# Optimization experiments

Hardware: AMD Instinct MI355X
Metric: run time of the kernel (lower is better)

## Reference

```python
import jax, jax.numpy as jnp
import numpy as np

B, T, E, NH, VOCAB, MULT = 1, 1024, 768, 12, 32000, 32
N = E * MULT // NH  # 2048
LN_EPS = 1e-5


def setup_inputs() -> dict:
    key = jax.random.key(0)
    ks = jax.random.split(key, 6)
    return {
        "idx": jax.random.randint(ks[0], (B, T), 0, VOCAB),
        "embed": jax.random.normal(ks[1], (VOCAB, E), jnp.float32) * 0.02,
        "encoder": jax.random.normal(ks[2], (NH, E, N), jnp.float32) * 0.02,
        "encoder_v": jax.random.normal(ks[3], (NH, E, N), jnp.float32) * 0.02,
        "decoder": jax.random.normal(ks[4], (NH * N, E), jnp.float32) * 0.02,
        "lm_head": jax.random.normal(ks[5], (VOCAB, E), jnp.float32) * 0.02,
        "ln_w": jnp.ones((E,), jnp.float32),
        "ln_b": jnp.zeros((E,), jnp.float32),
        "n_layer": 6,
    }


def reference(idx, embed, encoder, encoder_v, decoder, lm_head, ln_w, ln_b, n_layer):
    nh, e, n = encoder.shape
    t = idx.shape[1]
    dec = decoder.reshape(nh, n, e)  # flatten order (h, n) -> h*N + n

    def ln(x):
        m = jnp.mean(x, axis=-1, keepdims=True)
        v = jnp.mean(jnp.square(x - m), axis=-1, keepdims=True)
        return (x - m) * jax.lax.rsqrt(v + LN_EPS) * ln_w + ln_b

    causal = jnp.tril(jnp.ones((t, t), bool))  # [T, T]
    scale = 1.0 / np.sqrt(n).astype(np.float32)

    x = ln(embed[idx])  # [B, T, E]  (the unsqueezed head dim broadcasts; keep it squeezed)
    for _ in range(n_layer):
        # encoder projection + ReLU: [B,T,E] x [H,E,N] -> [B,H,T,N]
        x_sparse = jax.nn.relu(jnp.einsum("bte,hen->bhtn", x, encoder))
        # hand-rolled causal attention, Q=K=x_sparse, V=x (broadcast over heads)
        scores = jnp.einsum("bhqn,bhkn->bhqk", x_sparse, x_sparse) * scale
        scores = jnp.where(causal, scores, -jnp.inf)
        attn = jax.nn.softmax(scores, axis=-1)
        y = jnp.einsum("bhqk,bke->bhqe", attn, x)  # [B,H,T,E]
        y = ln(y)
        y_sparse = jax.nn.relu(jnp.einsum("bhte,hen->bhtn", y, encoder_v))
        xy = x_sparse * y_sparse  # [B,H,T,N]; dropout p=0 -> identity
        y_mlp = jnp.einsum("bhtn,hne->bte", xy, dec)  # decoder matmul
        x = ln(x + ln(y_mlp))
    logits = jnp.einsum("bte,ve->btv", x, lm_head)
    return logits
```

## Files before the change

kernel.cpp:

```cpp
#include <hip/hip_runtime.h>

typedef unsigned short u16;
typedef short bf16x8 __attribute__((ext_vector_type(8)));
typedef float f32x4 __attribute__((ext_vector_type(4)));
typedef u16 u16x4 __attribute__((ext_vector_type(4)));

#define TT     1024
#define EE     768
#define NHH    12
#define ND     2048
#define VOC    32000
#define HNN    24576
#define NLAYER 6
#define LN_EPS 1e-5f
#define SPLITK 16

__device__ __forceinline__ float b2f(u16 u){
  unsigned int x = ((unsigned int)u) << 16; float f; __builtin_memcpy(&f, &x, 4); return f;
}
__device__ __forceinline__ u16 f2b(float f){
  unsigned int x; __builtin_memcpy(&x, &f, 4);
  x = x + 0x7fffu + ((x >> 16) & 1u);
  return (u16)(x >> 16);
}

__device__ __forceinline__ void gload16(const void* g, void* lds){
  __builtin_amdgcn_global_load_lds(
      (const __attribute__((address_space(1))) unsigned int*)g,
      (__attribute__((address_space(3))) unsigned int*)(unsigned int)(unsigned long long)lds,
      16, 0, 0);
}

__device__ __forceinline__ bf16x8 ldsr(unsigned addr){
  bf16x8 r;
  asm volatile("ds_read_b128 %0, %1" : "=v"(r) : "v"(addr));
  return r;
}

__device__ __forceinline__ void blk_sum2(float& a, float& b){
  #pragma unroll
  for (int o = 32; o > 0; o >>= 1){ a += __shfl_down(a, o); b += __shfl_down(b, o); }
  __shared__ float sa[4], sb[4];
  int lane = threadIdx.x & 63, wid = threadIdx.x >> 6;
  __syncthreads();
  if (lane == 0){ sa[wid] = a; sb[wid] = b; }
  __syncthreads();
  a = (sa[0] + sa[1]) + (sa[2] + sa[3]);
  b = (sb[0] + sb[1]) + (sb[2] + sb[3]);
}
__device__ __forceinline__ float blk_max(float v){
  #pragma unroll
  for (int o = 32; o > 0; o >>= 1) v = fmaxf(v, __shfl_down(v, o));
  __shared__ float sm[4];
  int lane = threadIdx.x & 63, wid = threadIdx.x >> 6;
  __syncthreads();
  if (lane == 0) sm[wid] = v;
  __syncthreads();
  return fmaxf(fmaxf(sm[0], sm[1]), fmaxf(sm[2], sm[3]));
}
__device__ __forceinline__ float blk_sum(float v){
  #pragma unroll
  for (int o = 32; o > 0; o >>= 1) v += __shfl_down(v, o);
  __shared__ float ss[4];
  int lane = threadIdx.x & 63, wid = threadIdx.x >> 6;
  __syncthreads();
  if (lane == 0) ss[wid] = v;
  __syncthreads();
  return (ss[0] + ss[1]) + (ss[2] + ss[3]);
}

__global__ void transpose_f2b(const float* __restrict__ in, long sIn,
                              u16* __restrict__ out, long sOut, int R, int Cc){
  __shared__ float tile[32][33];
  int z = blockIdx.z;
  in  += (long)z * sIn;
  out += (long)z * sOut;
  int c0 = blockIdx.x * 32, r0 = blockIdx.y * 32;
  int lx = threadIdx.x & 31, ly = threadIdx.x >> 5;
  #pragma unroll
  for (int i = 0; i < 32; i += 8)
    tile[ly + i][lx] = in[(long)(r0 + ly + i) * Cc + (c0 + lx)];
  __syncthreads();
  #pragma unroll
  for (int i = 0; i < 32; i += 8)
    out[(long)(c0 + ly + i) * R + (r0 + lx)] = f2b(tile[lx][ly + i]);
}

__global__ void conv_f2b(const float* __restrict__ in, u16* __restrict__ out){
  long i = ((long)blockIdx.x * 256 + threadIdx.x) * 4;
  float4 v = *(const float4*)(in + i);
  u16x4 o; o.x = f2b(v.x); o.y = f2b(v.y); o.z = f2b(v.z); o.w = f2b(v.w);
  *(u16x4*)(out + i) = o;
}

__global__ void embed_ln(const int* __restrict__ idx, const float* __restrict__ emb,
                         const float* __restrict__ w, const float* __restrict__ b,
                         float* __restrict__ xf, u16* __restrict__ xb, u16* __restrict__ xT){
  int t = blockIdx.x, tid = threadIdx.x;
  const float* src = emb + (long)idx[t] * EE;
  float v[3];
  #pragma unroll
  for (int j = 0; j < 3; j++) v[j] = src[tid + j * 256];
  float s = v[0] + v[1] + v[2];
  float s2 = v[0]*v[0] + v[1]*v[1] + v[2]*v[2];
  blk_sum2(s, s2);
  float m  = s * (1.0f / EE);
  float var = s2 * (1.0f / EE) - m * m;
  float rs = rsqrtf(var + LN_EPS);
  #pragma unroll
  for (int j = 0; j < 3; j++){
    int e = tid + j * 256;
    float o = (v[j] - m) * rs * w[e] + b[e];
    xf[(long)t * EE + e] = o;
    u16 ob = f2b(o);
    xb[(long)t * EE + e] = ob;
    xT[(long)e * TT + t] = ob;
  }
}

__global__ void ln_rows(const float* __restrict__ in, u16* __restrict__ out,
                        const float* __restrict__ w, const float* __restrict__ b){
  long row = blockIdx.x; int tid = threadIdx.x;
  const float* src = in + row * EE;
  float v[3];
  #pragma unroll
  for (int j = 0; j < 3; j++) v[j] = src[tid + j * 256];
  float s = v[0] + v[1] + v[2];
  float s2 = v[0]*v[0] + v[1]*v[1] + v[2]*v[2];
  blk_sum2(s, s2);
  float m = s * (1.0f / EE);
  float var = s2 * (1.0f / EE) - m * m;
  float rs = rsqrtf(var + LN_EPS);
  #pragma unroll
  for (int j = 0; j < 3; j++){
    int e = tid + j * 256;
    out[row * EE + e] = f2b((v[j] - m) * rs * w[e] + b[e]);
  }
}

__global__ void softmax_rows(const float* __restrict__ scores, u16* __restrict__ attn){
  int q = blockIdx.x, h = blockIdx.y, tid = threadIdx.x;
  const float* srow = scores + ((long)h * TT + q) * TT;
  u16* arow = attn + ((long)h * TT + q) * TT;
  const int len = q + 1;
  const int pad = (q + 128) & ~127;
  float v[4];
  float mx = -1e30f;
  #pragma unroll
  for (int j = 0; j < 4; j++){
    int i = tid + j * 256;
    if (i < len){ v[j] = srow[i]; mx = fmaxf(mx, v[j]); }
  }
  mx = blk_max(mx);
  float s = 0.f;
  #pragma unroll
  for (int j = 0; j < 4; j++){
    int i = tid + j * 256;
    if (i < len){ v[j] = __expf(v[j] - mx); s += v[j]; }
  }
  float inv = 1.0f / blk_sum(s);
  #pragma unroll
  for (int j = 0; j < 4; j++){
    int i = tid + j * 256;
    if (i < pad){
      u16 o = 0;
      if (i < len) o = f2b(v[j] * inv);
      arow[i] = o;
    }
  }
}

template<int P>
__global__ void residual_ln(const u16* __restrict__ part, const float* __restrict__ xin,
                            float* __restrict__ xf, u16* __restrict__ xb, u16* __restrict__ xT,
                            const float* __restrict__ w, const float* __restrict__ b){
  int t = blockIdx.x, tid = threadIdx.x;
  float g[3];
  #pragma unroll
  for (int j = 0; j < 3; j++){
    int e = tid + j * 256;
    float s = 0.f;
    #pragma unroll
    for (int pp = 0; pp < P; pp++) s += b2f(part[((long)pp * TT + t) * EE + e]);
    g[j] = s;
  }
  float s = g[0] + g[1] + g[2], s2 = g[0]*g[0] + g[1]*g[1] + g[2]*g[2];
  blk_sum2(s, s2);
  float m = s * (1.0f / EE), var = s2 * (1.0f / EE) - m * m;
  float rs = rsqrtf(var + LN_EPS);
  float hh[3];
  #pragma unroll
  for (int j = 0; j < 3; j++){
    int e = tid + j * 256;
    hh[j] = xin[(long)t * EE + e] + ((g[j] - m) * rs * w[e] + b[e]);
  }
  s = hh[0] + hh[1] + hh[2]; s2 = hh[0]*hh[0] + hh[1]*hh[1] + hh[2]*hh[2];
  blk_sum2(s, s2);
  m = s * (1.0f / EE); var = s2 * (1.0f / EE) - m * m; rs = rsqrtf(var + LN_EPS);
  #pragma unroll
  for (int j = 0; j < 3; j++){
    int e = tid + j * 256;
    float o = (hh[j] - m) * rs * w[e] + b[e];
    xf[(long)t * EE + e] = o;
    u16 ob = f2b(o);
    xb[(long)t * EE + e] = ob;
    xT[(long)e * TT + t] = ob;
  }
}

template<int EPI>
__global__ __launch_bounds__(512, 2)
void g8(const u16* __restrict__ Ab, long sA,
        const u16* __restrict__ Bb, long sB,
        void* __restrict__ Cb, long sC,
        int grid_m, int grid_mn,
        int K, int lda, int ldb, int ldc, float scale,
        const u16* __restrict__ Mul, long sMul, int ldmul){
  __shared__ __align__(16) u16 S[69632];

  const int nwg = gridDim.x, orig = blockIdx.x;
  const int q = nwg >> 3, r = nwg & 7, xcd = orig & 7;
  const int wgid = (xcd < r ? xcd*(q+1) : r*(q+1) + (xcd - r)*q) + (orig >> 3);
  const int z   = wgid / grid_mn;
  const int rem = wgid - z*grid_mn;
  const int nb  = rem / grid_m;
  const int mb  = rem - nb*grid_m;
  const int m0 = mb*256, n0 = nb*256;
  const int tid = threadIdx.x, lane = tid & 63, wid = tid >> 6;

  if (EPI == 2 && n0 > m0 + 255) return;

  const u16* A = Ab + (long)z*sA;
  const u16* B = Bb + (long)z*sB;

  const int rS = wid*16 + (lane >> 2);
  const int cS = (((lane & 3) ^ ((rS >> 1) & 3)) << 3);
  const u16* gA = A + (long)(m0 + rS)*lda + cS;
  const u16* gB = B + (long)(n0 + rS)*ldb + cS;

  char* Sb = (char*)&S[0];
  const unsigned db0 = 0, db1 = 65536u, scr = 131072u;
  auto issue = [&](const u16* src, unsigned dstOff){
    gload16(src, Sb + dstOff + (unsigned)wid*1024u);
  };

  const int wr = wid >> 2, wc = wid & 3;
  const int fr = lane & 15, fk = lane >> 4;
  const unsigned base = (unsigned)(unsigned long long)Sb;
  unsigned aOff[8], bOff[4];
  #pragma unroll
  for (int mi = 0; mi < 8; mi++){
    int row = wr*128 + mi*16 + fr;
    aOff[mi] = (unsigned)(row*64 + ((fk ^ ((row >> 1) & 3)) << 4));
  }
  #pragma unroll
  for (int ni = 0; ni < 4; ni++){
    int row = wc*64 + ni*16 + fr;
    bOff[ni] = 32768u + (unsigned)(row*64 + ((fk ^ ((row >> 1) & 3)) << 4));
  }

  const int NT = K >> 6;
  const long lda128 = (long)128*lda, ldb128 = (long)128*ldb;

  f32x4 acc[8][4] = {};

  issue(gA,              db0);          issue(gA + lda128,          db0 + 8192u);
  issue(gB,              db0+32768u);   issue(gB + ldb128,          db0 + 40960u);
  issue(gA + 32,         db0+16384u);   issue(gA + 32 + lda128,     db0 + 24576u);
  issue(gB + 32,         db0+49152u);   issue(gB + 32 + ldb128,     db0 + 57344u);
  issue(gA + 64,         db1);          issue(gA + 64 + lda128,     db1 + 8192u);
  issue(gB + 64,         db1+32768u);   issue(gB + 64 + ldb128,     db1 + 40960u);
  asm volatile("s_waitcnt vmcnt(8)" ::: "memory");
  __builtin_amdgcn_s_barrier();
  __builtin_amdgcn_sched_barrier(0);

  for (int t = 0; t < NT; t++){
    const unsigned cur = (t & 1) ? db1 : db0;
    const unsigned oth = (t & 1) ? db0 : db1;
    const bool v1 = (t + 1 < NT), v2 = (t + 2 < NT);
    const long k1 = (long)(v1 ? t + 1 : 0) * 64;
    const long k2 = (long)(v2 ? t + 2 : 0) * 64;
    const unsigned d1A = v1 ? oth + 16384u : scr;
    const unsigned d1B = v1 ? oth + 49152u : scr;
    const unsigned d2A = v2 ? cur           : scr;
    const unsigned d2B = v2 ? cur + 32768u  : scr;
    bf16x8 a[4], b[4];

    #pragma unroll
    for (int ni = 0; ni < 4; ni++) b[ni] = ldsr(base + cur + bOff[ni]);
    #pragma unroll
    for (int u = 0; u < 4; u++)    a[u]  = ldsr(base + cur + aOff[u]);
    issue(gA + k1 + 32, d1A); issue(gA + k1 + 32 + lda128, d1A + 8192u);
    __builtin_amdgcn_s_barrier();
    asm volatile("s_waitcnt lgkmcnt(0)" ::: "memory");
    __builtin_amdgcn_sched_barrier(0);
    __builtin_amdgcn_s_setprio(1);
    #pragma unroll
    for (int u = 0; u < 4; u++)
      #pragma unroll
      for (int ni = 0; ni < 4; ni++)
        acc[u][ni] = __builtin_amdgcn_mfma_f32_16x16x32_bf16(a[u], b[ni], acc[u][ni], 0, 0, 0);
    __builtin_amdgcn_s_setprio(0);
    __builtin_amdgcn_s_barrier();
    __builtin_amdgcn_sched_barrier(0);

    #pragma unroll
    for (int u = 0; u < 4; u++) a[u] = ldsr(base + cur + aOff[4 + u]);
    issue(gB + k1 + 32, d1B); issue(gB + k1 + 32 + ldb128, d1B + 8192u);
    __builtin_amdgcn_s_barrier();
    asm volatile("s_waitcnt lgkmcnt(0)" ::: "memory");
    __builtin_amdgcn_sched_barrier(0);
    __builtin_amdgcn_s_setprio(1);
    #pragma unroll
    for (int u = 0; u < 4; u++)
      #pragma unroll
      for (int ni = 0; ni < 4; ni++)
        acc[4+u][ni] = __builtin_amdgcn_mfma_f32_16x16x32_bf16(a[u], b[ni], acc[4+u][ni], 0, 0, 0);
    __builtin_amdgcn_s_setprio(0);
    asm volatile("s_waitcnt vmcnt(8)" ::: "memory");
    __builtin_amdgcn_s_barrier();
    __builtin_amdgcn_sched_barrier(0);

    #pragma unroll
    for (int ni = 0; ni < 4; ni++) b[ni] = ldsr(base + cur + bOff[ni] + 16384u);
    #pragma unroll
    for (int u = 0; u < 4; u++)    a[u]  = ldsr(base + cur + aOff[u] + 16384u);
    issue(gA + k2, d2A); issue(gA + k2 + lda128, d2A + 8192u);
    __builtin_amdgcn_s_barrier();
    asm volatile("s_waitcnt lgkmcnt(0)" ::: "memory");
    __builtin_amdgcn_sched_barrier(0);
    __builtin_amdgcn_s_setprio(1);
    #pragma unroll
    for (int u = 0; u < 4; u++)
      #pragma unroll
      for (int ni = 0; ni < 4; ni++)
        acc[u][ni] = __builtin_amdgcn_mfma_f32_16x16x32_bf16(a[u], b[ni], acc[u][ni], 0, 0, 0);
    __builtin_amdgcn_s_setprio(0);
    __builtin_amdgcn_s_barrier();
    __builtin_amdgcn_sched_barrier(0);

    #pragma unroll
    for (int u = 0; u < 4; u++) a[u] = ldsr(base + cur + aOff[4 + u] + 16384u);
    issue(gB + k2, d2B); issue(gB + k2 + ldb128, d2B + 8192u);
    __builtin_amdgcn_s_barrier();
    asm volatile("s_waitcnt lgkmcnt(0)" ::: "memory");
    __builtin_amdgcn_sched_barrier(0);
    __builtin_amdgcn_s_setprio(1);
    #pragma unroll
    for (int u = 0; u < 4; u++)
      #pragma unroll
      for (int ni = 0; ni < 4; ni++)
        acc[4+u][ni] = __builtin_amdgcn_mfma_f32_16x16x32_bf16(a[u], b[ni], acc[4+u][ni], 0, 0, 0);
    __builtin_amdgcn_s_setprio(0);
    asm volatile("s_waitcnt vmcnt(8)" ::: "memory");
    __builtin_amdgcn_s_barrier();
    __builtin_amdgcn_sched_barrier(0);
  }
  asm volatile("s_waitcnt vmcnt(0)" ::: "memory");

  const int er = (lane >> 4) * 4, ec = lane & 15;
  #pragma unroll
  for (int mi = 0; mi < 8; mi++){
    #pragma unroll
    for (int ni = 0; ni < 4; ni++){
      #pragma unroll
      for (int j = 0; j < 4; j++){
        int row = m0 + wr*128 + mi*16 + er + j;
        int col = n0 + wc*64 + ni*16 + ec;
        float v = acc[mi][ni][j];
        if (EPI == 0){
          ((float*)Cb + (long)z * sC)[(long)row * ldc + col] = v;
        } else if (EPI == 1){
          v = v > 0.f ? v : 0.f;
          ((u16*)Cb + (long)z * sC)[(long)row * ldc + col] = f2b(v);
        } else if (EPI == 2){
          ((float*)Cb + (long)z * sC)[(long)row * ldc + col] = v * scale;
        } else {
          v = v > 0.f ? v : 0.f;
          float mfv = b2f((Mul + (long)z * sMul)[(long)row * ldmul + col]);
          ((u16*)Cb + (long)z * sC)[(long)row * ldc + col] = f2b(v * mfv);
        }
      }
    }
  }
}

template<int EPI, bool CCLAMP>
__global__ __launch_bounds__(256, 2)
void gemmw(const u16* __restrict__ Ab, long sA,
           const u16* __restrict__ Bb, long sB,
           void* __restrict__ Cb, long sC,
           int grid_m, int grid_mn,
           int K, int lda, int ldb, int ldc){
  constexpr unsigned BUFB = 24576u;
  __shared__ __align__(16) u16 S[3 * 12288];

  const int nwg = gridDim.x, orig = blockIdx.x;
  const int q = nwg >> 3, r = nwg & 7, xcd = orig & 7;
  const int wgid = (xcd < r ? xcd*(q+1) : r*(q+1) + (xcd - r)*q) + (orig >> 3);
  const int z   = wgid / grid_mn;
  const int rem = wgid - z*grid_mn;
  const int nb  = rem / grid_m;
  const int mb  = rem - nb*grid_m;
  const int m0 = mb*128, n0 = nb*256;
  const int tid = threadIdx.x, lane = tid & 63, wid = tid >> 6;

  const u16* A = Ab + (long)z*sA;
  const u16* B = Bb + (long)z*sB;

  const int rS = tid >> 2;
  const int cS = (((tid & 3) ^ ((rS >> 1) & 3)) << 3);
  const u16* gA[2]; const u16* gB[4];
  #pragma unroll
  for (int i = 0; i < 2; i++) gA[i] = A + (long)(m0 + i*64 + rS)*lda + cS;
  #pragma unroll
  for (int i = 0; i < 4; i++) gB[i] = B + (long)(n0 + i*64 + rS)*ldb + cS;

  char* Sb = (char*)&S[0];
  auto stage = [&](int kt, unsigned bB){
    const int ko = kt << 5;
    gload16(gA[0] + ko, Sb + bB +          wid*1024u);
    gload16(gA[1] + ko, Sb + bB +  4096u + wid*1024u);
    #pragma unroll
    for (int i = 0; i < 4; i++)
      gload16(gB[i] + ko, Sb + bB + 8192u + i*4096u + wid*1024u);
  };

  const int wr = wid >> 1, wc = wid & 1;
  const int fr = lane & 15, fk = lane >> 4;
  const unsigned base = (unsigned)(unsigned long long)Sb;
  unsigned aAd[4], bAd[8];
  #pragma unroll
  for (int mi = 0; mi < 4; mi++){
    int row = wr*64 + mi*16 + fr;
    aAd[mi] = base + (unsigned)(row*64 + ((fk ^ ((row >> 1) & 3)) << 4));
  }
  #pragma unroll
  for (int ni = 0; ni < 8; ni++){
    int row = wc*128 + ni*16 + fr;
    bAd[ni] = base + 8192u + (unsigned)(row*64 + ((fk ^ ((row >> 1) & 3)) << 4));
  }

  const int Keff = CCLAMP ? (m0 + 128 < K ? m0 + 128 : K) : K;
  const int NT = Keff >> 5;
  const int s0 = (mb*13 + nb*7 + z*5) % NT;

  f32x4 acc[4][8] = {};

  int p1 = s0 + 1; if (p1 >= NT) p1 -= NT;
  stage(s0, 0);
  stage(p1, BUFB);
  asm volatile("s_waitcnt vmcnt(6)" ::: "memory");
  __builtin_amdgcn_s_barrier();
  __builtin_amdgcn_sched_barrier(0);

  unsigned rbB = 0, wbB = 2u*BUFB;
  for (int t = 0; t < NT; t++){
    int nx = (t + 2 < NT) ? t + 2 : NT - 1;
    int ph = s0 + nx; if (ph >= NT) ph -= NT;
    stage(ph, wbB);
    bf16x8 afr[4], bfr[8];
    #pragma unroll
    for (int ni = 0; ni < 8; ni++) bfr[ni] = ldsr(bAd[ni] + rbB);
    #pragma unroll
    for (int mi = 0; mi < 4; mi++) afr[mi] = ldsr(aAd[mi] + rbB);
    __builtin_amdgcn_s_barrier();
    asm volatile("s_waitcnt lgkmcnt(0)" ::: "memory");
    __builtin_amdgcn_sched_barrier(0);
    __builtin_amdgcn_s_setprio(1);
    #pragma unroll
    for (int mi = 0; mi < 4; mi++)
      #pragma unroll
      for (int ni = 0; ni < 8; ni++)
        acc[mi][ni] = __builtin_amdgcn_mfma_f32_16x16x32_bf16(afr[mi], bfr[ni], acc[mi][ni], 0, 0, 0);
    __builtin_amdgcn_s_setprio(0);
    __builtin_amdgcn_sched_barrier(0);
    asm volatile("s_waitcnt vmcnt(6)" ::: "memory");
    __builtin_amdgcn_s_barrier();
    __builtin_amdgcn_sched_barrier(0);
    unsigned tmp = rbB; rbB += BUFB; if (rbB == 3u*BUFB) rbB = 0;
    wbB = tmp;
  }
  asm volatile("s_waitcnt vmcnt(0)" ::: "memory");

  const int er = (lane >> 4) * 4, ec = lane & 15;
  #pragma unroll
  for (int mi = 0; mi < 4; mi++){
    #pragma unroll
    for (int ni = 0; ni < 8; ni++){
      #pragma unroll
      for (int j = 0; j < 4; j++){
        int row = m0 + wr*64 + mi*16 + er + j;
        int col = n0 + wc*128 + ni*16 + ec;
        float v = acc[mi][ni][j];
        if (EPI == 0){
          ((float*)Cb + (long)z * sC)[(long)row * ldc + col] = v;
        } else {
          ((u16*)Cb + (long)z * sC)[(long)row * ldc + col] = f2b(v);
        }
      }
    }
  }
}

extern "C" void kernel_launch(void* const* d_in, const int* in_sizes, int n_in,
                              void* d_out, int out_size, void* d_ws, size_t ws_size,
                              hipStream_t stream){
  (void)in_sizes; (void)n_in; (void)out_size; (void)ws_size;
  const int*   idx     = (const int*)  d_in[0];
  const float* embed   = (const float*)d_in[1];
  const float* encoder = (const float*)d_in[2];
  const float* encv    = (const float*)d_in[3];
  const float* decoder = (const float*)d_in[4];
  const float* lm_head = (const float*)d_in[5];
  const float* ln_w    = (const float*)d_in[6];
  const float* ln_b    = (const float*)d_in[7];
  float* out = (float*)d_out;

  char* p = (char*)d_ws;
  auto take = [&](size_t n){ char* r = p; p += (n + 255) & ~(size_t)255; return r; };
  u16*   encT  = (u16*)  take((size_t)NHH * ND * EE * 2);
  u16*   encvT = (u16*)  take((size_t)NHH * ND * EE * 2);
  u16*   decT  = (u16*)  take((size_t)EE * HNN * 2);
  u16*   lmhB  = (u16*)  take((size_t)VOC * EE * 2);
  float* xf    = (float*)take((size_t)TT * EE * 4);
  u16*   xb    = (u16*)  take((size_t)TT * EE * 2);
  u16*   xT    = (u16*)  take((size_t)EE * TT * 2);
  u16*   xs    = (u16*)  take((size_t)NHH * TT * ND * 2);
  char*  big   =         take((size_t)NHH * TT * TT * 4);
  u16*   attn  = (u16*)  take((size_t)NHH * TT * TT * 2);
  u16*   yb    = (u16*)  take((size_t)NHH * TT * EE * 2);
  take((size_t)8 * TT * EE * 4);
  float* scores = (float*)big;
  float* yf     = (float*)big;
  u16*   xy     = (u16*)big;
  u16*   part   = attn;

  dim3 blk(256, 1, 1);

  transpose_f2b<<<dim3(ND / 32, EE / 32, NHH), blk, 0, stream>>>(encoder, (long)EE * ND, encT,  (long)ND * EE, EE, ND);
  transpose_f2b<<<dim3(ND / 32, EE / 32, NHH), blk, 0, stream>>>(encv,    (long)EE * ND, encvT, (long)ND * EE, EE, ND);
  transpose_f2b<<<dim3(EE / 32, HNN / 32, 1),  blk, 0, stream>>>(decoder, 0, decT, 0, HNN, EE);
  conv_f2b<<<dim3((VOC * EE) / 1024, 1, 1), blk, 0, stream>>>(lm_head, lmhB);

  embed_ln<<<dim3(TT, 1, 1), blk, 0, stream>>>(idx, embed, ln_w, ln_b, xf, xb, xT);

  const float scl = 0.022097086912079608f;

  for (int L = 0; L < NLAYER; ++L){
    g8<1><<<dim3(4*8*NHH), dim3(512), 0, stream>>>(
        xb, 0, encT, (long)ND * EE, xs, (long)TT * ND,
        4, 32, EE, EE, EE, ND, 0.f, (const u16*)0, 0, 0);
    g8<2><<<dim3(4*4*NHH), dim3(512), 0, stream>>>(
        xs, (long)TT * ND, xs, (long)TT * ND, scores, (long)TT * TT,
        4, 16, ND, ND, ND, TT, scl, (const u16*)0, 0, 0);
    softmax_rows<<<dim3(TT, NHH, 1), blk, 0, stream>>>(scores, attn);
    gemmw<0,true><<<dim3(8*3*NHH), blk, 0, stream>>>(
        attn, (long)TT * TT, xT, 0, yf, (long)TT * EE,
        8, 24, TT, TT, TT, EE);
    ln_rows<<<dim3(NHH * TT, 1, 1), blk, 0, stream>>>(yf, yb, ln_w, ln_b);
    g8<3><<<dim3(4*8*NHH), dim3(512), 0, stream>>>(
        yb, (long)TT * EE, encvT, (long)ND * EE, xy, (long)ND,
        4, 32, EE, EE, EE, HNN, 0.f, xs, (long)TT * ND, ND);
    gemmw<4,false><<<dim3(8*3*SPLITK), blk, 0, stream>>>(
        xy, (long)(HNN / SPLITK), decT, (long)(HNN / SPLITK), part, (long)TT * EE,
        8, 24, HNN / SPLITK, HNN, HNN, EE);
    residual_ln<SPLITK><<<dim3(TT, 1, 1), blk, 0, stream>>>(part, xf, xf, xb, xT, ln_w, ln_b);
  }

  g8<0><<<dim3(4*125), dim3(512), 0, stream>>>(
      xb, 0, lmhB, 0, out, 0,
      4, 500, EE, EE, EE, VOC, 0.f, (const u16*)0, 0, 0);
}
```

Baseline: 1.964 ms.

## Store scores and attention outputs in bf16 and transpose x with a tiled kernel

Attention scores are now written by the score GEMM as bf16 instead of fp32, and softmax reads bf16. The attn@x GEMM writes bf16 through the EPI 4 path, and ln_rows reads it, halving that intermediate's traffic. The strided scattered xT writes in embed_ln and residual_ln are replaced by a separate LDS-tiled transpose kernel. This cuts memory bandwidth on the large per-head intermediates, but it adds precision loss in the scores before softmax and in the pre-LN activations, plus one extra launch per layer.

```diff
diff --git a/kernel.cpp b/kernel.cpp
--- a/kernel.cpp
+++ b/kernel.cpp
@@ -93,9 +93,22 @@
   *(u16x4*)(out + i) = o;
 }
 
+__global__ void xpose(const u16* __restrict__ in, u16* __restrict__ out){
+  __shared__ u16 t[64][65];
+  int e0 = blockIdx.x * 64, t0 = blockIdx.y * 64;
+  int lx = threadIdx.x & 63, ly = threadIdx.x >> 6;
+  #pragma unroll
+  for (int i = 0; i < 64; i += 4)
+    t[ly + i][lx] = in[(long)(t0 + ly + i) * EE + e0 + lx];
+  __syncthreads();
+  #pragma unroll
+  for (int i = 0; i < 64; i += 4)
+    out[(long)(e0 + ly + i) * TT + t0 + lx] = t[lx][ly + i];
+}
+
 __global__ void embed_ln(const int* __restrict__ idx, const float* __restrict__ emb,
                          const float* __restrict__ w, const float* __restrict__ b,
-                         float* __restrict__ xf, u16* __restrict__ xb, u16* __restrict__ xT){
+                         float* __restrict__ xf, u16* __restrict__ xb){
   int t = blockIdx.x, tid = threadIdx.x;
   const float* src = emb + (long)idx[t] * EE;
   float v[3];
@@ -112,19 +125,17 @@
     int e = tid + j * 256;
     float o = (v[j] - m) * rs * w[e] + b[e];
     xf[(long)t * EE + e] = o;
-    u16 ob = f2b(o);
-    xb[(long)t * EE + e] = ob;
-    xT[(long)e * TT + t] = ob;
-  }
-}
-
-__global__ void ln_rows(const float* __restrict__ in, u16* __restrict__ out,
+    xb[(long)t * EE + e] = f2b(o);
+  }
+}
+
+__global__ void ln_rows(const u16* __restrict__ in, u16* __restrict__ out,
                         const float* __restrict__ w, const float* __restrict__ b){
   long row = blockIdx.x; int tid = threadIdx.x;
-  const float* src = in + row * EE;
+  const u16* src = in + row * EE;
   float v[3];
   #pragma unroll
-  for (int j = 0; j < 3; j++) v[j] = src[tid + j * 256];
+  for (int j = 0; j < 3; j++) v[j] = b2f(src[tid + j * 256]);
   float s = v[0] + v[1] + v[2];
   float s2 = v[0]*v[0] + v[1]*v[1] + v[2]*v[2];
   blk_sum2(s, s2);
@@ -138,9 +149,9 @@
   }
 }
 
-__global__ void softmax_rows(const float* __restrict__ scores, u16* __restrict__ attn){
+__global__ void softmax_rows(const u16* __restrict__ scores, u16* __restrict__ attn){
   int q = blockIdx.x, h = blockIdx.y, tid = threadIdx.x;
-  const float* srow = scores + ((long)h * TT + q) * TT;
+  const u16* srow = scores + ((long)h * TT + q) * TT;
   u16* arow = attn + ((long)h * TT + q) * TT;
   const int len = q + 1;
   const int pad = (q + 128) & ~127;
@@ -149,7 +160,7 @@
   #pragma unroll
   for (int j = 0; j < 4; j++){
     int i = tid + j * 256;
-    if (i < len){ v[j] = srow[i]; mx = fmaxf(mx, v[j]); }
+    if (i < len){ v[j] = b2f(srow[i]); mx = fmaxf(mx, v[j]); }
   }
   mx = blk_max(mx);
   float s = 0.f;
@@ -172,7 +183,7 @@
 
 template<int P>
 __global__ void residual_ln(const u16* __restrict__ part, const float* __restrict__ xin,
-                            float* __restrict__ xf, u16* __restrict__ xb, u16* __restrict__ xT,
+                            float* __restrict__ xf, u16* __restrict__ xb,
                             const float* __restrict__ w, const float* __restrict__ b){
   int t = blockIdx.x, tid = threadIdx.x;
   float g[3];
@@ -202,9 +213,7 @@
     int e = tid + j * 256;
     float o = (hh[j] - m) * rs * w[e] + b[e];
     xf[(long)t * EE + e] = o;
-    u16 ob = f2b(o);
-    xb[(long)t * EE + e] = ob;
-    xT[(long)e * TT + t] = ob;
+    xb[(long)t * EE + e] = f2b(o);
   }
 }
 
@@ -374,7 +383,7 @@
           v = v > 0.f ? v : 0.f;
           ((u16*)Cb + (long)z * sC)[(long)row * ldc + col] = f2b(v);
         } else if (EPI == 2){
-          ((float*)Cb + (long)z * sC)[(long)row * ldc + col] = v * scale;
+          ((u16*)Cb + (long)z * sC)[(long)row * ldc + col] = f2b(v * scale);
         } else {
           v = v > 0.f ? v : 0.f;
           float mfv = b2f((Mul + (long)z * sMul)[(long)row * ldmul + col]);
@@ -531,8 +540,8 @@
   u16*   attn  = (u16*)  take((size_t)NHH * TT * TT * 2);
   u16*   yb    = (u16*)  take((size_t)NHH * TT * EE * 2);
   take((size_t)8 * TT * EE * 4);
-  float* scores = (float*)big;
-  float* yf     = (float*)big;
+  u16*   scores = (u16*)big;
+  u16*   ybig   = (u16*)big;
   u16*   xy     = (u16*)big;
   u16*   part   = attn;
 
@@ -543,7 +552,8 @@
   transpose_f2b<<<dim3(EE / 32, HNN / 32, 1),  blk, 0, stream>>>(decoder, 0, decT, 0, HNN, EE);
   conv_f2b<<<dim3((VOC * EE) / 1024, 1, 1), blk, 0, stream>>>(lm_head, lmhB);
 
-  embed_ln<<<dim3(TT, 1, 1), blk, 0, stream>>>(idx, embed, ln_w, ln_b, xf, xb, xT);
+  embed_ln<<<dim3(TT, 1, 1), blk, 0, stream>>>(idx, embed, ln_w, ln_b, xf, xb);
+  xpose<<<dim3(EE / 64, TT / 64, 1), blk, 0, stream>>>(xb, xT);
 
   const float scl = 0.022097086912079608f;
 
@@ -555,17 +565,18 @@
         xs, (long)TT * ND, xs, (long)TT * ND, scores, (long)TT * TT,
         4, 16, ND, ND, ND, TT, scl, (const u16*)0, 0, 0);
     softmax_rows<<<dim3(TT, NHH, 1), blk, 0, stream>>>(scores, attn);
-    gemmw<0,true><<<dim3(8*3*NHH), blk, 0, stream>>>(
-        attn, (long)TT * TT, xT, 0, yf, (long)TT * EE,
+    gemmw<4,true><<<dim3(8*3*NHH), blk, 0, stream>>>(
+        attn, (long)TT * TT, xT, 0, ybig, (long)TT * EE,
         8, 24, TT, TT, TT, EE);
-    ln_rows<<<dim3(NHH * TT, 1, 1), blk, 0, stream>>>(yf, yb, ln_w, ln_b);
+    ln_rows<<<dim3(NHH * TT, 1, 1), blk, 0, stream>>>(ybig, yb, ln_w, ln_b);
     g8<3><<<dim3(4*8*NHH), dim3(512), 0, stream>>>(
         yb, (long)TT * EE, encvT, (long)ND * EE, xy, (long)ND,
         4, 32, EE, EE, EE, HNN, 0.f, xs, (long)TT * ND, ND);
     gemmw<4,false><<<dim3(8*3*SPLITK), blk, 0, stream>>>(
         xy, (long)(HNN / SPLITK), decT, (long)(HNN / SPLITK), part, (long)TT * EE,
         8, 24, HNN / SPLITK, HNN, HNN, EE);
-    residual_ln<SPLITK><<<dim3(TT, 1, 1), blk, 0, stream>>>(part, xf, xf, xb, xT, ln_w, ln_b);
+    residual_ln<SPLITK><<<dim3(TT, 1, 1), blk, 0, stream>>>(part, xf, xf, xb, ln_w, ln_b);
+    xpose<<<dim3(EE / 64, TT / 64, 1), blk, 0, stream>>>(xb, xT);
   }
 
   g8<0><<<dim3(4*125), dim3(512), 0, stream>>>(
```

Measured after the change: 1.927 ms. About the same (-1.9%).
